# Kernel optimization log

Hardware: AMD Instinct MI355X
Metric: run time of the kernel (lower is better)

Reference implementation:

```python
import jax, jax.numpy as jnp
import numpy as np
from functools import partial

TAU = 2.0
V_TH = 1.0
T_STEPS = 10
SG_ALPHA = 4.0  # spikingjelly surrogate.Sigmoid default

@jax.custom_vjp
def spike(x):
    # Heaviside: 1 where x >= 0 (spikingjelly heaviside semantics)
    return (x >= 0).astype(x.dtype)

def _spike_fwd(x):
    return spike(x), x

def _spike_bwd(x, g):
    s = jax.nn.sigmoid(SG_ALPHA * x)
    return (g * SG_ALPHA * s * (1.0 - s),)

spike.defvjp(_spike_fwd, _spike_bwd)

def setup_inputs() -> dict:
    key = jax.random.key(0)
    ks = jax.random.split(key, 7)
    B, D_IN, H, A = 4096, 2048, 2048, 5
    def lin(k, fan_in, shape):
        bound = 1.0 / np.sqrt(fan_in)
        return jax.random.uniform(k, shape, jnp.float32, -bound, bound)
    return {
        "x": jax.random.normal(ks[0], (B, D_IN), jnp.float32),
        "W_in": lin(ks[1], D_IN, (D_IN, H)),
        "b_in": lin(ks[2], D_IN, (H,)),
        "W_snn": lin(ks[3], H, (H, H)),
        "b_snn": lin(ks[4], H, (H,)),
        "W_out": lin(ks[5], H, (H, A)),
        "b_out": lin(ks[6], H, (A,)),
    }

def lif_step(v, cur):
    # decay_input=True, v_reset=0: v <- v + (I - v)/tau; hard reset with detached spike
    v = v + (cur - v) / TAU
    s = spike(v - V_TH)
    v = (1.0 - jax.lax.stop_gradient(s)) * v
    return v, s

def reference(x, W_in, b_in, W_snn, b_snn, W_out, b_out):
    # input projection [B, H]
    h = x @ W_in + b_in
    # RSNNBlock: fc(h) is the same every timestep; LIF state carries across T steps
    cur = h @ W_snn + b_snn
    v0 = jnp.zeros_like(cur)
    _, spikes = jax.lax.scan(lambda v, _: lif_step(v, cur), v0, None, length=T_STEPS)
    rate = spikes.mean(axis=0)  # [B, H], mean firing rate
    # output head + single-step output LIF (fresh state v=0)
    pre = rate @ W_out + b_out  # [B, A]
    v_out, s_out = lif_step(jnp.zeros_like(pre), pre)
    return s_out
```

## Files before the change

### kernel.cpp

```cpp
#include <hip/hip_runtime.h>
#include <hip/hip_bf16.h>

static constexpr int BATCH = 4096;
static constexpr int DIN   = 2048;
static constexpr int HDIM  = 2048;
static constexpr int ADIM  = 5;
static constexpr int TSTEPS = 10;

typedef __attribute__((ext_vector_type(8))) short short8;
typedef __attribute__((ext_vector_type(4))) float floatx4;

__device__ __forceinline__ unsigned short f2bf(float f) {
  unsigned int u = __float_as_uint(f);
  unsigned int r = (u + 0x7fffu + ((u >> 16) & 1u)) >> 16;
  return (unsigned short)r;
}
__device__ __forceinline__ float bf2f(unsigned short u) {
  return __uint_as_float(((unsigned int)u) << 16);
}

__global__ __launch_bounds__(256) void k_cvt(const float4* __restrict__ in,
                                             ushort4* __restrict__ out, int n4) {
  int i = blockIdx.x * 256 + threadIdx.x;
  if (i < n4) {
    float4 v = in[i];
    ushort4 o;
    o.x = f2bf(v.x); o.y = f2bf(v.y); o.z = f2bf(v.z); o.w = f2bf(v.w);
    out[i] = o;
  }
}

__global__ __launch_bounds__(256) void k_transpose_cvt(const float* __restrict__ in,
                                                       unsigned short* __restrict__ out,
                                                       int n) {
  __shared__ float tl[32][33];
  int c0 = blockIdx.x * 32, r0 = blockIdx.y * 32;
  int tx = threadIdx.x, ty = threadIdx.y;
  #pragma unroll
  for (int s = 0; s < 32; s += 8)
    tl[ty + s][tx] = in[(size_t)(r0 + ty + s) * n + (c0 + tx)];
  __syncthreads();
  #pragma unroll
  for (int s = 0; s < 32; s += 8)
    out[(size_t)(c0 + ty + s) * n + (r0 + tx)] = f2bf(tl[tx][ty + s]);
}

template <int MODE>
__global__ __launch_bounds__(256) void k_gemm(const unsigned short* __restrict__ Ag,
                                              const unsigned short* __restrict__ BTg,
                                              const float* __restrict__ bias,
                                              unsigned short* __restrict__ outb,
                                              int M, int N, int K) {
  constexpr int BM = 128, BN = 128, BK = 64;
  __shared__ unsigned short Al[BM * BK];
  __shared__ unsigned short Bl[BN * BK];

  const int nbn = N / BN;
  const int nwg = gridDim.x;
  const int wg = blockIdx.x;
  const int cpx = nwg >> 3;
  const int swz = (wg & 7) * cpx + (wg >> 3);
  const int bm = swz / nbn, bn = swz % nbn;
  const int m0 = bm * BM, n0 = bn * BN;

  const int t = threadIdx.x;
  const int l = t & 63;
  const int w = t >> 6;
  const int wrow = w >> 1, wcol = w & 1;

  const int srow = t >> 3;
  const int scol = (((t & 7) ^ ((t >> 3) & 7)) << 3);
  const unsigned short* gA = Ag + (size_t)(m0 + srow) * K + scol;
  const unsigned short* gB = BTg + (size_t)(n0 + srow) * K + scol;

  const int slotbase = (l >> 4) ^ (l & 7);
  const int baseA = (wrow * 64 + (l & 15)) * 128;
  const int baseB = (wcol * 64 + (l & 15)) * 128;

  floatx4 acc[4][4] = {};

  for (int kt = 0; kt < K; kt += BK) {
    __syncthreads();
    #pragma unroll
    for (int j = 0; j < 4; ++j) {
      __builtin_amdgcn_global_load_lds(
          (const __attribute__((address_space(1))) void*)(gA + (size_t)j * 32 * K + kt),
          (__attribute__((address_space(3))) void*)((char*)Al + t * 16 + j * 4096),
          16, 0, 0);
    }
    #pragma unroll
    for (int j = 0; j < 4; ++j) {
      __builtin_amdgcn_global_load_lds(
          (const __attribute__((address_space(1))) void*)(gB + (size_t)j * 32 * K + kt),
          (__attribute__((address_space(3))) void*)((char*)Bl + t * 16 + j * 4096),
          16, 0, 0);
    }
    __syncthreads();

    #pragma unroll
    for (int kkb = 0; kkb <= 4; kkb += 4) {
      short8 af[4], bfr[4];
      const int so = ((kkb ^ slotbase) << 4);
      #pragma unroll
      for (int i = 0; i < 4; ++i)
        af[i] = *(const short8*)((const char*)Al + baseA + i * 2048 + so);
      #pragma unroll
      for (int i = 0; i < 4; ++i)
        bfr[i] = *(const short8*)((const char*)Bl + baseB + i * 2048 + so);
      #pragma unroll
      for (int i = 0; i < 4; ++i)
        #pragma unroll
        for (int jj = 0; jj < 4; ++jj)
          acc[i][jj] = __builtin_amdgcn_mfma_f32_16x16x32_bf16(af[i], bfr[jj],
                                                               acc[i][jj], 0, 0, 0);
    }
  }

  const int crow = m0 + wrow * 64 + ((l >> 4) << 2);
  const int ccol = n0 + wcol * 64 + (l & 15);
  #pragma unroll
  for (int jj = 0; jj < 4; ++jj) {
    const int col = ccol + jj * 16;
    const float bv = bias[col];
    #pragma unroll
    for (int i = 0; i < 4; ++i) {
      const int row = crow + i * 16;
      #pragma unroll
      for (int r = 0; r < 4; ++r) {
        float v = acc[i][jj][r] + bv;
        if (MODE == 1) {
          float vm = 0.f;
          int cnt = 0;
          #pragma unroll
          for (int s = 0; s < TSTEPS; ++s) {
            vm = vm + (v - vm) * 0.5f;
            int sp = (vm - 1.0f >= 0.0f) ? 1 : 0;
            cnt += sp;
            vm = sp ? 0.0f : vm;
          }
          v = (float)cnt;
        }
        outb[(size_t)(row + r) * N + col] = f2bf(v);
      }
    }
  }
}

__global__ __launch_bounds__(256) void k_head(const unsigned short* __restrict__ cntb,
                                              const float* __restrict__ Wout,
                                              const float* __restrict__ bout,
                                              float* __restrict__ out) {
  __shared__ float Wl[HDIM * ADIM];
  const int t = threadIdx.x;
  for (int i = t; i < HDIM * ADIM; i += 256) Wl[i] = Wout[i];
  __syncthreads();
  const int w = t >> 6, l = t & 63;
  const int row = blockIdx.x * 4 + w;
  const unsigned short* rp = cntb + (size_t)row * HDIM;
  float acc[ADIM] = {};
  #pragma unroll
  for (int it = 0; it < 4; ++it) {
    const int k0 = it * 512 + l * 8;
    short8 v = *(const short8*)(rp + k0);
    #pragma unroll
    for (int jj = 0; jj < 8; ++jj) {
      const float c = bf2f((unsigned short)v[jj]);
      const int k = k0 + jj;
      #pragma unroll
      for (int a = 0; a < ADIM; ++a) acc[a] += c * Wl[k * ADIM + a];
    }
  }
  #pragma unroll
  for (int a = 0; a < ADIM; ++a)
    #pragma unroll
    for (int off = 32; off >= 1; off >>= 1)
      acc[a] += __shfl_down(acc[a], off, 64);
  if (l == 0) {
    #pragma unroll
    for (int a = 0; a < ADIM; ++a) {
      const float pre = acc[a] * 0.1f + bout[a];
      const float vout = pre * 0.5f;
      out[(size_t)row * ADIM + a] = (vout - 1.0f >= 0.0f) ? 1.0f : 0.0f;
    }
  }
}

extern "C" void kernel_launch(void* const* d_in, const int* in_sizes, int n_in,
                              void* d_out, int out_size, void* d_ws, size_t ws_size,
                              hipStream_t stream) {
  const float* x     = (const float*)d_in[0];
  const float* W_in  = (const float*)d_in[1];
  const float* b_in  = (const float*)d_in[2];
  const float* W_snn = (const float*)d_in[3];
  const float* b_snn = (const float*)d_in[4];
  const float* W_out = (const float*)d_in[5];
  const float* b_out = (const float*)d_in[6];
  float* out = (float*)d_out;

  char* ws = (char*)d_ws;
  unsigned short* xb   = (unsigned short*)(ws);
  unsigned short* WinT = (unsigned short*)(ws + (size_t)16 * 1024 * 1024);
  unsigned short* WsnT = (unsigned short*)(ws + (size_t)24 * 1024 * 1024);
  unsigned short* hb   = (unsigned short*)(ws + (size_t)32 * 1024 * 1024);
  unsigned short* cntb = xb;

  const int n4 = BATCH * DIN / 4;
  k_cvt<<<(n4 + 255) / 256, 256, 0, stream>>>((const float4*)x, (ushort4*)xb, n4);

  dim3 tb(32, 8);
  dim3 tg(DIN / 32, HDIM / 32);
  k_transpose_cvt<<<tg, tb, 0, stream>>>(W_in, WinT, DIN);
  k_transpose_cvt<<<tg, tb, 0, stream>>>(W_snn, WsnT, HDIM);

  const int gblk = (BATCH / 128) * (HDIM / 128);
  k_gemm<0><<<gblk, 256, 0, stream>>>(xb, WinT, b_in, hb, BATCH, HDIM, DIN);

  k_gemm<1><<<gblk, 256, 0, stream>>>(hb, WsnT, b_snn, cntb, BATCH, HDIM, HDIM);

  k_head<<<BATCH / 4, 256, 0, stream>>>(cntb, W_out, b_out, out);
}
```

Before: 220.3 us.

## Triple-buffer GEMM with 256x128 tiles, 512 threads, and closed-form LIF spike count

Reworks the bf16 MFMA GEMM to use 256x128 tiles with 8 waves and a three-stage LDS ring, so global-to-LDS loads for tile t+2 overlap MFMA work on tile t. Waits use explicit vmcnt counts, and barriers plus s_setprio interleave loads with compute. The 10-step LIF loop in the epilogue is replaced by threshold comparisons that give the same spike count. The larger LDS footprint (72KB per block) and 512 threads may limit occupancy.

```diff
diff --git a/kernel.cpp b/kernel.cpp
--- a/kernel.cpp
+++ b/kernel.cpp
@@ -5,7 +5,6 @@
 static constexpr int DIN   = 2048;
 static constexpr int HDIM  = 2048;
 static constexpr int ADIM  = 5;
-static constexpr int TSTEPS = 10;
 
 typedef __attribute__((ext_vector_type(8))) short short8;
 typedef __attribute__((ext_vector_type(4))) float floatx4;
@@ -46,18 +45,18 @@
 }
 
 template <int MODE>
-__global__ __launch_bounds__(256) void k_gemm(const unsigned short* __restrict__ Ag,
-                                              const unsigned short* __restrict__ BTg,
-                                              const float* __restrict__ bias,
-                                              unsigned short* __restrict__ outb,
-                                              int M, int N, int K) {
-  constexpr int BM = 128, BN = 128, BK = 64;
-  __shared__ unsigned short Al[BM * BK];
-  __shared__ unsigned short Bl[BN * BK];
+__global__ __launch_bounds__(512, 2) void k_gemm(const unsigned short* __restrict__ Ag,
+                                                 const unsigned short* __restrict__ BTg,
+                                                 const float* __restrict__ bias,
+                                                 unsigned short* __restrict__ outb,
+                                                 int M, int N, int K) {
+  constexpr int BM = 256, BN = 128, BK = 64;
+  __shared__ unsigned short Al[3][BM * BK];
+  __shared__ unsigned short Bl[3][BN * BK];
 
   const int nbn = N / BN;
   const int nwg = gridDim.x;
-  const int wg = blockIdx.x;
+  const int wg  = blockIdx.x;
   const int cpx = nwg >> 3;
   const int swz = (wg & 7) * cpx + (wg >> 3);
   const int bm = swz / nbn, bn = swz % nbn;
@@ -66,53 +65,79 @@
   const int t = threadIdx.x;
   const int l = t & 63;
   const int w = t >> 6;
-  const int wrow = w >> 1, wcol = w & 1;
+  const int wrow = w >> 1;
+  const int wcol = w & 1;
 
   const int srow = t >> 3;
-  const int scol = (((t & 7) ^ ((t >> 3) & 7)) << 3);
+  const int scol = (((t & 7) ^ (srow & 7)) << 3);
   const unsigned short* gA = Ag + (size_t)(m0 + srow) * K + scol;
   const unsigned short* gB = BTg + (size_t)(n0 + srow) * K + scol;
 
-  const int slotbase = (l >> 4) ^ (l & 7);
-  const int baseA = (wrow * 64 + (l & 15)) * 128;
-  const int baseB = (wcol * 64 + (l & 15)) * 128;
+  const int NT = K / BK;
+
+  auto stageA = [&](int tt) {
+    const int kt = tt * BK;
+    char* dst = (char*)&Al[tt % 3][0] + t * 16;
+    #pragma unroll
+    for (int j = 0; j < 4; ++j)
+      __builtin_amdgcn_global_load_lds(
+          (const __attribute__((address_space(1))) void*)(gA + (size_t)j * 64 * K + kt),
+          (__attribute__((address_space(3))) void*)(dst + j * 8192), 16, 0, 0);
+  };
+  auto stageB = [&](int tt) {
+    const int kt = tt * BK;
+    char* dst = (char*)&Bl[tt % 3][0] + t * 16;
+    #pragma unroll
+    for (int j = 0; j < 2; ++j)
+      __builtin_amdgcn_global_load_lds(
+          (const __attribute__((address_space(1))) void*)(gB + (size_t)j * 64 * K + kt),
+          (__attribute__((address_space(3))) void*)(dst + j * 8192), 16, 0, 0);
+  };
+
+  const int rA = wrow * 64 + (l & 15);
+  const int rB = wcol * 64 + (l & 15);
+  const int kl = l >> 4;
 
   floatx4 acc[4][4] = {};
 
-  for (int kt = 0; kt < K; kt += BK) {
-    __syncthreads();
-    #pragma unroll
-    for (int j = 0; j < 4; ++j) {
-      __builtin_amdgcn_global_load_lds(
-          (const __attribute__((address_space(1))) void*)(gA + (size_t)j * 32 * K + kt),
-          (__attribute__((address_space(3))) void*)((char*)Al + t * 16 + j * 4096),
-          16, 0, 0);
-    }
-    #pragma unroll
-    for (int j = 0; j < 4; ++j) {
-      __builtin_amdgcn_global_load_lds(
-          (const __attribute__((address_space(1))) void*)(gB + (size_t)j * 32 * K + kt),
-          (__attribute__((address_space(3))) void*)((char*)Bl + t * 16 + j * 4096),
-          16, 0, 0);
-    }
-    __syncthreads();
-
-    #pragma unroll
-    for (int kkb = 0; kkb <= 4; kkb += 4) {
-      short8 af[4], bfr[4];
-      const int so = ((kkb ^ slotbase) << 4);
+  stageA(0); stageB(0);
+  stageA(1); stageB(1);
+  asm volatile("s_waitcnt vmcnt(6)" ::: "memory");
+  __builtin_amdgcn_s_barrier();
+
+  for (int tt = 0; tt < NT; ++tt) {
+    const unsigned short* Ab = &Al[tt % 3][0];
+    const unsigned short* Bb = &Bl[tt % 3][0];
+    const bool pre = (tt + 2 < NT);
+    #pragma unroll
+    for (int p = 0; p < 2; ++p) {
+      short8 af[4], bfv[4];
+      const int soA = ((((p << 2) | kl) ^ (rA & 7)) << 4);
+      const int soB = ((((p << 2) | kl) ^ (rB & 7)) << 4);
       #pragma unroll
       for (int i = 0; i < 4; ++i)
-        af[i] = *(const short8*)((const char*)Al + baseA + i * 2048 + so);
+        af[i] = *(const short8*)((const char*)Ab + rA * 128 + i * 2048 + soA);
       #pragma unroll
       for (int i = 0; i < 4; ++i)
-        bfr[i] = *(const short8*)((const char*)Bl + baseB + i * 2048 + so);
+        bfv[i] = *(const short8*)((const char*)Bb + rB * 128 + i * 2048 + soB);
+      if (p == 0) { if (pre) stageA(tt + 2); }
+      else        { if (pre) stageB(tt + 2); }
+      __builtin_amdgcn_s_barrier();
+      __builtin_amdgcn_s_setprio(1);
       #pragma unroll
       for (int i = 0; i < 4; ++i)
         #pragma unroll
         for (int jj = 0; jj < 4; ++jj)
-          acc[i][jj] = __builtin_amdgcn_mfma_f32_16x16x32_bf16(af[i], bfr[jj],
+          acc[i][jj] = __builtin_amdgcn_mfma_f32_16x16x32_bf16(af[i], bfv[jj],
                                                                acc[i][jj], 0, 0, 0);
+      __builtin_amdgcn_s_setprio(0);
+      if (p == 0) {
+        __builtin_amdgcn_s_barrier();
+      } else {
+        if (tt + 2 < NT)      asm volatile("s_waitcnt vmcnt(6)" ::: "memory");
+        else if (tt + 1 < NT) asm volatile("s_waitcnt vmcnt(0)" ::: "memory");
+        if (tt + 1 < NT) __builtin_amdgcn_s_barrier();
+      }
     }
   }
 
@@ -129,16 +154,13 @@
       for (int r = 0; r < 4; ++r) {
         float v = acc[i][jj][r] + bv;
         if (MODE == 1) {
-          float vm = 0.f;
-          int cnt = 0;
-          #pragma unroll
-          for (int s = 0; s < TSTEPS; ++s) {
-            vm = vm + (v - vm) * 0.5f;
-            int sp = (vm - 1.0f >= 0.0f) ? 1 : 0;
-            cnt += sp;
-            vm = sp ? 0.0f : vm;
-          }
-          v = (float)cnt;
+          float c;
+          c = (v >= 2.0f)                  ? 10.f
+            : (v >= 1.3333333333333333f)   ? 5.f
+            : (v >= 1.1428571428571428f)   ? 3.f
+            : (v >= 1.0322580645161290f)   ? 2.f
+            : (v >= 1.0009775171065494f)   ? 1.f : 0.f;
+          v = c;
         }
         outb[(size_t)(row + r) * N + col] = f2bf(v);
       }
@@ -212,10 +234,10 @@
   k_transpose_cvt<<<tg, tb, 0, stream>>>(W_in, WinT, DIN);
   k_transpose_cvt<<<tg, tb, 0, stream>>>(W_snn, WsnT, HDIM);
 
-  const int gblk = (BATCH / 128) * (HDIM / 128);
-  k_gemm<0><<<gblk, 256, 0, stream>>>(xb, WinT, b_in, hb, BATCH, HDIM, DIN);
-
-  k_gemm<1><<<gblk, 256, 0, stream>>>(hb, WsnT, b_snn, cntb, BATCH, HDIM, HDIM);
+  const int gblk = (BATCH / 256) * (HDIM / 128);
+  k_gemm<0><<<gblk, 512, 0, stream>>>(xb, WinT, b_in, hb, BATCH, HDIM, DIN);
+
+  k_gemm<1><<<gblk, 512, 0, stream>>>(hb, WsnT, b_snn, cntb, BATCH, HDIM, HDIM);
 
   k_head<<<BATCH / 4, 256, 0, stream>>>(cntb, W_out, b_out, out);
 }
```

Result: faster. 211.7 us (-3.9%).

## Double-buffer GEMM LDS, split K across waves, merge prep kernels, closed-form spike count

Applied to the files above, without the earlier changes.

Merges the three conversion and transpose kernels into one launch. Restructures the GEMM with double-buffered LDS so the next tile's global loads overlap the current tile's MFMAs. Each wave pair now splits the BK slice along K and the partial sums are reduced through LDS in the epilogue. The 10-step LIF loop is replaced by threshold comparisons that give the spike count directly. The change costs more accumulator registers and LDS, and adds an extra epilogue reduction in exchange for less launch overhead and better latency hiding.

```diff
diff --git a/kernel.cpp b/kernel.cpp
--- a/kernel.cpp
+++ b/kernel.cpp
@@ -5,7 +5,6 @@
 static constexpr int DIN   = 2048;
 static constexpr int HDIM  = 2048;
 static constexpr int ADIM  = 5;
-static constexpr int TSTEPS = 10;
 
 typedef __attribute__((ext_vector_type(8))) short short8;
 typedef __attribute__((ext_vector_type(4))) float floatx4;
@@ -19,128 +18,161 @@
   return __uint_as_float(((unsigned int)u) << 16);
 }
 
-__global__ __launch_bounds__(256) void k_cvt(const float4* __restrict__ in,
-                                             ushort4* __restrict__ out, int n4) {
-  int i = blockIdx.x * 256 + threadIdx.x;
-  if (i < n4) {
-    float4 v = in[i];
+__global__ __launch_bounds__(256) void k_prep(const float* __restrict__ x,
+                                              const float* __restrict__ W_in,
+                                              const float* __restrict__ W_snn,
+                                              unsigned short* __restrict__ xb,
+                                              unsigned short* __restrict__ WinT,
+                                              unsigned short* __restrict__ WsnT) {
+  __shared__ float tl[32][33];
+  const int b = blockIdx.x;
+  if (b < 8192) {
+    const int i = b * 256 + threadIdx.x;
+    float4 v = ((const float4*)x)[i];
     ushort4 o;
     o.x = f2bf(v.x); o.y = f2bf(v.y); o.z = f2bf(v.z); o.w = f2bf(v.w);
-    out[i] = o;
-  }
-}
-
-__global__ __launch_bounds__(256) void k_transpose_cvt(const float* __restrict__ in,
-                                                       unsigned short* __restrict__ out,
-                                                       int n) {
-  __shared__ float tl[32][33];
-  int c0 = blockIdx.x * 32, r0 = blockIdx.y * 32;
-  int tx = threadIdx.x, ty = threadIdx.y;
-  #pragma unroll
-  for (int s = 0; s < 32; s += 8)
-    tl[ty + s][tx] = in[(size_t)(r0 + ty + s) * n + (c0 + tx)];
-  __syncthreads();
-  #pragma unroll
-  for (int s = 0; s < 32; s += 8)
-    out[(size_t)(c0 + ty + s) * n + (r0 + tx)] = f2bf(tl[tx][ty + s]);
+    ((ushort4*)xb)[i] = o;
+  } else {
+    int bi = b - 8192;
+    const float* src;
+    unsigned short* dst;
+    if (bi < 4096) { src = W_in; dst = WinT; }
+    else           { src = W_snn; dst = WsnT; bi -= 4096; }
+    const int bx = bi & 63, by = bi >> 6;
+    const int c0 = bx * 32, r0 = by * 32;
+    const int tx = threadIdx.x & 31, ty = threadIdx.x >> 5;
+    #pragma unroll
+    for (int s = 0; s < 32; s += 8)
+      tl[ty + s][tx] = src[(size_t)(r0 + ty + s) * 2048 + (c0 + tx)];
+    __syncthreads();
+    #pragma unroll
+    for (int s = 0; s < 32; s += 8)
+      dst[(size_t)(c0 + ty + s) * 2048 + (r0 + tx)] = f2bf(tl[tx][ty + s]);
+  }
 }
 
 template <int MODE>
-__global__ __launch_bounds__(256) void k_gemm(const unsigned short* __restrict__ Ag,
-                                              const unsigned short* __restrict__ BTg,
-                                              const float* __restrict__ bias,
-                                              unsigned short* __restrict__ outb,
-                                              int M, int N, int K) {
-  constexpr int BM = 128, BN = 128, BK = 64;
-  __shared__ unsigned short Al[BM * BK];
-  __shared__ unsigned short Bl[BN * BK];
-
-  const int nbn = N / BN;
+__global__ __launch_bounds__(256, 2) void k_gemm(const unsigned short* __restrict__ Ag,
+                                                 const unsigned short* __restrict__ BTg,
+                                                 const float* __restrict__ bias,
+                                                 unsigned short* __restrict__ outb,
+                                                 int M, int N, int K) {
+  constexpr int BK = 64;
+  __shared__ unsigned short smem[2][16384];
+
+  const int nbn = N / 128;
   const int nwg = gridDim.x;
-  const int wg = blockIdx.x;
+  const int wg  = blockIdx.x;
   const int cpx = nwg >> 3;
   const int swz = (wg & 7) * cpx + (wg >> 3);
   const int bm = swz / nbn, bn = swz % nbn;
-  const int m0 = bm * BM, n0 = bn * BN;
+  const int m0 = bm * 128, n0 = bn * 128;
 
   const int t = threadIdx.x;
   const int l = t & 63;
   const int w = t >> 6;
-  const int wrow = w >> 1, wcol = w & 1;
+  const int wc  = w & 1;
+  const int kkh = w >> 1;
 
   const int srow = t >> 3;
-  const int scol = (((t & 7) ^ ((t >> 3) & 7)) << 3);
-  const unsigned short* gA = Ag + (size_t)(m0 + srow) * K + scol;
-  const unsigned short* gB = BTg + (size_t)(n0 + srow) * K + scol;
-
-  const int slotbase = (l >> 4) ^ (l & 7);
-  const int baseA = (wrow * 64 + (l & 15)) * 128;
-  const int baseB = (wcol * 64 + (l & 15)) * 128;
-
-  floatx4 acc[4][4] = {};
-
-  for (int kt = 0; kt < K; kt += BK) {
-    __syncthreads();
-    #pragma unroll
-    for (int j = 0; j < 4; ++j) {
+  const int sg = (((t & 7) ^ (srow & 7)) << 3);
+  const unsigned short* gA = Ag + (size_t)(m0 + srow) * K + sg;
+  const unsigned short* gB = BTg + (size_t)(n0 + srow) * K + sg;
+
+  const int NT = K / BK;
+
+  auto stage = [&](int tt) {
+    const int kt = tt * BK;
+    char* base = (char*)&smem[tt & 1][0];
+    #pragma unroll
+    for (int j = 0; j < 4; ++j)
       __builtin_amdgcn_global_load_lds(
           (const __attribute__((address_space(1))) void*)(gA + (size_t)j * 32 * K + kt),
-          (__attribute__((address_space(3))) void*)((char*)Al + t * 16 + j * 4096),
-          16, 0, 0);
-    }
-    #pragma unroll
-    for (int j = 0; j < 4; ++j) {
+          (__attribute__((address_space(3))) void*)(base + t * 16 + j * 4096), 16, 0, 0);
+    #pragma unroll
+    for (int j = 0; j < 4; ++j)
       __builtin_amdgcn_global_load_lds(
           (const __attribute__((address_space(1))) void*)(gB + (size_t)j * 32 * K + kt),
-          (__attribute__((address_space(3))) void*)((char*)Bl + t * 16 + j * 4096),
-          16, 0, 0);
+          (__attribute__((address_space(3))) void*)(base + 16384 + t * 16 + j * 4096), 16, 0, 0);
+  };
+
+  const int soff = (((kkh << 2) | (l >> 4)) ^ (l & 7)) << 4;
+  const int rA0 = (l & 15) * 128;
+  const int rB0 = (wc * 64 + (l & 15)) * 128;
+
+  floatx4 acc[8][4] = {};
+
+  stage(0);
+  __syncthreads();
+
+  for (int tt = 0; tt < NT; ++tt) {
+    if (tt + 1 < NT) stage(tt + 1);
+    const char* Ab = (const char*)&smem[tt & 1][0];
+    const char* Bb = Ab + 32768;
+    short8 bf[4];
+    #pragma unroll
+    for (int j = 0; j < 4; ++j)
+      bf[j] = *(const short8*)(Bb + rB0 + j * 2048 + soff);
+    {
+      short8 af[4];
+      #pragma unroll
+      for (int i = 0; i < 4; ++i)
+        af[i] = *(const short8*)(Ab + rA0 + i * 2048 + soff);
+      #pragma unroll
+      for (int i = 0; i < 4; ++i)
+        #pragma unroll
+        for (int j = 0; j < 4; ++j)
+          acc[i][j] = __builtin_amdgcn_mfma_f32_16x16x32_bf16(af[i], bf[j],
+                                                              acc[i][j], 0, 0, 0);
+    }
+    {
+      short8 af[4];
+      #pragma unroll
+      for (int i = 0; i < 4; ++i)
+        af[i] = *(const short8*)(Ab + rA0 + (i + 4) * 2048 + soff);
+      #pragma unroll
+      for (int i = 0; i < 4; ++i)
+        #pragma unroll
+        for (int j = 0; j < 4; ++j)
+          acc[i + 4][j] = __builtin_amdgcn_mfma_f32_16x16x32_bf16(af[i], bf[j],
+                                                                  acc[i + 4][j], 0, 0, 0);
     }
     __syncthreads();
-
-    #pragma unroll
-    for (int kkb = 0; kkb <= 4; kkb += 4) {
-      short8 af[4], bfr[4];
-      const int so = ((kkb ^ slotbase) << 4);
-      #pragma unroll
-      for (int i = 0; i < 4; ++i)
-        af[i] = *(const short8*)((const char*)Al + baseA + i * 2048 + so);
-      #pragma unroll
-      for (int i = 0; i < 4; ++i)
-        bfr[i] = *(const short8*)((const char*)Bl + baseB + i * 2048 + so);
-      #pragma unroll
-      for (int i = 0; i < 4; ++i)
+  }
+
+  floatx4* xch = (floatx4*)&smem[0][0];
+  if (kkh == 1) {
+    #pragma unroll
+    for (int i = 0; i < 8; ++i)
+      #pragma unroll
+      for (int j = 0; j < 4; ++j)
+        xch[wc * 2048 + (i * 4 + j) * 64 + l] = acc[i][j];
+  }
+  __syncthreads();
+  if (kkh == 0) {
+    const int crow = m0 + ((l >> 4) << 2);
+    const int ccol = n0 + wc * 64 + (l & 15);
+    #pragma unroll
+    for (int j = 0; j < 4; ++j) {
+      const int col = ccol + j * 16;
+      const float bv = bias[col];
+      #pragma unroll
+      for (int i = 0; i < 8; ++i) {
+        floatx4 a = acc[i][j];
+        floatx4 o = xch[wc * 2048 + (i * 4 + j) * 64 + l];
+        const int row = crow + i * 16;
         #pragma unroll
-        for (int jj = 0; jj < 4; ++jj)
-          acc[i][jj] = __builtin_amdgcn_mfma_f32_16x16x32_bf16(af[i], bfr[jj],
-                                                               acc[i][jj], 0, 0, 0);
-    }
-  }
-
-  const int crow = m0 + wrow * 64 + ((l >> 4) << 2);
-  const int ccol = n0 + wcol * 64 + (l & 15);
-  #pragma unroll
-  for (int jj = 0; jj < 4; ++jj) {
-    const int col = ccol + jj * 16;
-    const float bv = bias[col];
-    #pragma unroll
-    for (int i = 0; i < 4; ++i) {
-      const int row = crow + i * 16;
-      #pragma unroll
-      for (int r = 0; r < 4; ++r) {
-        float v = acc[i][jj][r] + bv;
-        if (MODE == 1) {
-          float vm = 0.f;
-          int cnt = 0;
-          #pragma unroll
-          for (int s = 0; s < TSTEPS; ++s) {
-            vm = vm + (v - vm) * 0.5f;
-            int sp = (vm - 1.0f >= 0.0f) ? 1 : 0;
-            cnt += sp;
-            vm = sp ? 0.0f : vm;
+        for (int r = 0; r < 4; ++r) {
+          float v = a[r] + o[r] + bv;
+          if (MODE == 1) {
+            v = (v >= 2.0f)                ? 10.f
+              : (v >= 1.3333333333333333f) ? 5.f
+              : (v >= 1.1428571428571428f) ? 3.f
+              : (v >= 1.0322580645161290f) ? 2.f
+              : (v >= 1.0009775171065494f) ? 1.f : 0.f;
           }
-          v = (float)cnt;
+          outb[(size_t)(row + r) * N + col] = f2bf(v);
         }
-        outb[(size_t)(row + r) * N + col] = f2bf(v);
       }
     }
   }
@@ -204,13 +236,7 @@
   unsigned short* hb   = (unsigned short*)(ws + (size_t)32 * 1024 * 1024);
   unsigned short* cntb = xb;
 
-  const int n4 = BATCH * DIN / 4;
-  k_cvt<<<(n4 + 255) / 256, 256, 0, stream>>>((const float4*)x, (ushort4*)xb, n4);
-
-  dim3 tb(32, 8);
-  dim3 tg(DIN / 32, HDIM / 32);
-  k_transpose_cvt<<<tg, tb, 0, stream>>>(W_in, WinT, DIN);
-  k_transpose_cvt<<<tg, tb, 0, stream>>>(W_snn, WsnT, HDIM);
+  k_prep<<<16384, 256, 0, stream>>>(x, W_in, W_snn, xb, WinT, WsnT);
 
   const int gblk = (BATCH / 128) * (HDIM / 128);
   k_gemm<0><<<gblk, 256, 0, stream>>>(xb, WinT, b_in, hb, BATCH, HDIM, DIN);
```

After: 199.3 us. 1.11x faster.
